# Performance work log

Measured on AMD Instinct MI355X. Metric: run time of the kernel, lower is better.

Reference implementation:

```python
import jax, jax.numpy as jnp
import numpy as np

AT_ID = 5       # tokenizer id of '@'
CITSEG_ID = 7   # tokenizer id of 'CITSEG'


def setup_inputs() -> dict:
    key = jax.random.key(0)
    ks = jax.random.split(key, 12)
    B, S, H = 256, 512, 768
    CIT, D, NC = 750, 1518, 6
    s = lambda n: 1.0 / np.sqrt(n)
    return {
        "tokens": jax.random.randint(ks[0], (B, S), 0, 100),
        "hidden_states": jax.random.normal(ks[1], (B, S, H), jnp.float32),
        "proj_w": jax.random.normal(ks[2], (H, CIT), jnp.float32) * s(H),
        "proj_b": jax.random.normal(ks[3], (CIT,), jnp.float32) * 0.02,
        "enc_w": jax.random.normal(ks[4], (CIT, CIT), jnp.float32) * s(CIT),
        "enc_b": jax.random.normal(ks[5], (CIT,), jnp.float32) * 0.02,
        "w1": jax.random.normal(ks[6], (D, 2 * D), jnp.float32) * s(D),
        "b1": jax.random.normal(ks[7], (2 * D,), jnp.float32) * 0.02,
        "w2": jax.random.normal(ks[8], (2 * D, 2 * D), jnp.float32) * s(2 * D),
        "b2": jax.random.normal(ks[9], (2 * D,), jnp.float32) * 0.02,
        "w3": jax.random.normal(ks[10], (2 * D, NC), jnp.float32) * s(2 * D),
        "b3": jax.random.normal(ks[11], (NC,), jnp.float32) * 0.02,
    }


def _forward(tokens, hidden_states, proj_w, proj_b, enc_w, enc_b,
             w1, b1, w2, b2, w3, b3):
    B, S, H = hidden_states.shape
    idx = jnp.arange(S)[None, :]                       # [1,S]
    BIG = S + 1

    # --- ctx_pooler: masked max over tokens outside the [start,end] '@' span ---
    at_mask = tokens == AT_ID                          # [B,S]
    first = jnp.min(jnp.where(at_mask, idx, BIG), axis=1)            # [B]
    second = jnp.min(jnp.where(at_mask & (idx > first[:, None]), idx, BIG), axis=1)
    ge2 = at_mask.sum(axis=1) >= 2
    start = jnp.where(ge2, first, 0)
    end = jnp.where(ge2, second, S)                    # end=S excludes everything
    keep = (idx < start[:, None]) | (idx > end[:, None])             # [B,S]
    neg = jnp.finfo(hidden_states.dtype).min
    pooled = jnp.max(jnp.where(keep[:, :, None], hidden_states, neg), axis=1)  # [B,H]
    pooled = jnp.where(keep.any(axis=1)[:, None], pooled, 0.0)

    # --- CITSEG token gather + projection (zero row if absent) ---
    c_mask = tokens == CITSEG_ID
    c_first = jnp.min(jnp.where(c_mask, idx, BIG), axis=1)           # [B]
    has_c = c_mask.any(axis=1)
    safe_pos = jnp.minimum(c_first, S - 1)
    cit_h = jnp.take_along_axis(hidden_states, safe_pos[:, None, None], axis=1)[:, 0]  # [B,H]
    cit = (cit_h @ proj_w + proj_b) * has_c[:, None].astype(hidden_states.dtype)       # [B,750]

    # --- citseg_encoder (modeled as Linear 750->750) ---
    cit_enc = cit @ enc_w + enc_b

    # --- MLP head ---
    x = jnp.concatenate([pooled, cit_enc], axis=1)     # [B,1518]
    x = jax.nn.relu(x @ w1 + b1)
    x = jax.nn.relu(x @ w2 + b2)
    return x @ w3 + b3                                 # [B,num_class]


def reference(tokens, hidden_states, proj_w, proj_b, enc_w, enc_b,
              w1, b1, w2, b2, w3, b3):
    return _forward(tokens, hidden_states, proj_w, proj_b, enc_w, enc_b,
                    w1, b1, w2, b2, w3, b3)
```

## Files before the change

kernel.cpp:

```cpp
#include <hip/hip_runtime.h>
#include <hip/hip_bf16.h>

typedef __attribute__((ext_vector_type(8))) short bf16x8;
typedef __attribute__((ext_vector_type(4))) float f32x4;
typedef __attribute__((ext_vector_type(4))) unsigned short u16x4;

#define NEGINF (-3.4028234663852886e38f)

__device__ __forceinline__ unsigned short f2b(float f) {
    union { float f; unsigned u; } x; x.f = f;
    unsigned r = x.u + 0x7FFFu + ((x.u >> 16) & 1u);
    return (unsigned short)(r >> 16);
}
__device__ __forceinline__ float b2f(unsigned short b) {
    union { unsigned u; float f; } x; x.u = ((unsigned)b) << 16;
    return x.f;
}
__device__ __forceinline__ void load_lds16(const void* g, void* l) {
    __builtin_amdgcn_global_load_lds((const __attribute__((address_space(1))) void*)g,
                                     (__attribute__((address_space(3))) void*)l, 16, 0, 0);
}

__global__ __launch_bounds__(192) void scan_cit_k(const int* __restrict__ tokens,
                                                  const float* __restrict__ hs,
                                                  int* __restrict__ meta,
                                                  unsigned short* __restrict__ citA) {
    __shared__ int sm;
    const int S = 512, BIG = 1 << 20;
    int b = blockIdx.x, tid = threadIdx.x;
    if (tid < 64) {
        int l = tid;
        const int* row = tokens + (size_t)b * S;
        int base = l * 8;
        int toks[8];
#pragma unroll
        for (int i = 0; i < 8; ++i) toks[i] = row[base + i];
        int am = 0, cnt = 0, minAt = BIG, minC = BIG;
#pragma unroll
        for (int i = 0; i < 8; ++i) {
            if (toks[i] == 5) { am |= 1 << i; cnt++; if (base + i < minAt) minAt = base + i; }
            if (toks[i] == 7) { if (base + i < minC) minC = base + i; }
        }
        for (int off = 1; off < 64; off <<= 1) {
            minAt = min(minAt, __shfl_xor(minAt, off));
            minC  = min(minC,  __shfl_xor(minC,  off));
            cnt  += __shfl_xor(cnt, off);
        }
        int first = minAt, minAt2 = BIG;
#pragma unroll
        for (int i = 0; i < 8; ++i)
            if ((am >> i) & 1) { int idx = base + i; if (idx > first && idx < minAt2) minAt2 = idx; }
        for (int off = 1; off < 64; off <<= 1) minAt2 = min(minAt2, __shfl_xor(minAt2, off));
        if (l == 0) {
            int ge2 = (cnt >= 2) ? 1 : 0;
            int start = ge2 ? first : 0;
            int end = ge2 ? minAt2 : S;
            int anyKeep = (ge2 && (start > 0 || end < S - 1)) ? 1 : 0;
            int has_c = (minC < S) ? 1 : 0;
            int cpos = min(minC, S - 1);
            int* m = meta + b * 6;
            m[0] = start; m[1] = end; m[2] = cpos; m[3] = has_c; m[4] = anyKeep; m[5] = 0;
            sm = cpos;
        }
    }
    __syncthreads();
    int cpos = sm;
    f32x4 c = *(const f32x4*)(hs + ((size_t)b * 512 + cpos) * 768 + tid * 4);
    u16x4 co;
#pragma unroll
    for (int j = 0; j < 4; ++j) co[j] = f2b(c[j]);
    *(u16x4*)(citA + (size_t)b * 768 + tid * 4) = co;
}

__device__ __forceinline__ void trans32(const float* __restrict__ in, int K, int N,
                                        unsigned short* __restrict__ out, int ldo,
                                        int bx, int by, int tid, float (*tile)[33]) {
    int n0 = bx * 32, k0 = by * 32;
    int tx = tid & 31, ty = tid >> 5;
#pragma unroll
    for (int i = 0; i < 4; ++i) {
        int k = k0 + ty * 4 + i, n = n0 + tx;
        tile[ty * 4 + i][tx] = (k < K && n < N) ? in[(size_t)k * N + n] : 0.f;
    }
    __syncthreads();
    int n = tid >> 3, kc = tid & 7;
    u16x4 o;
#pragma unroll
    for (int q = 0; q < 4; ++q) o[q] = f2b(tile[kc * 4 + q][n]);
    *(u16x4*)(out + (size_t)(n0 + n) * ldo + k0 + kc * 4) = o;
}

__global__ __launch_bounds__(256) void pool_trans_k(
    const float* __restrict__ hs, const int* __restrict__ meta,
    float* __restrict__ part,
    const float* __restrict__ proj_w, const float* __restrict__ enc_w,
    const float* __restrict__ w1, const float* __restrict__ w2,
    unsigned short* __restrict__ projT, unsigned short* __restrict__ encT,
    unsigned short* __restrict__ w1T, unsigned short* __restrict__ w2T) {
    __shared__ float tile[32][33];
    int bid = blockIdx.x, tid = threadIdx.x;
    if (bid < 2048) {
        if (tid >= 192) return;
        int b = bid >> 3, ch = bid & 7;
        int start = meta[b * 6 + 0], end = meta[b * 6 + 1];
        f32x4 m = { NEGINF, NEGINF, NEGINF, NEGINF };
        const float* basep = hs + (size_t)b * 512 * 768 + tid * 4;
        int s0 = ch * 64, hi = s0 + 64;
        int e1 = min(start, hi);
        int s2 = max(end + 1, s0);
#pragma unroll 4
        for (int s = s0; s < e1; ++s) {
            f32x4 v = *(const f32x4*)(basep + (size_t)s * 768);
#pragma unroll
            for (int j = 0; j < 4; ++j) m[j] = fmaxf(m[j], v[j]);
        }
#pragma unroll 4
        for (int s = s2; s < hi; ++s) {
            f32x4 v = *(const f32x4*)(basep + (size_t)s * 768);
#pragma unroll
            for (int j = 0; j < 4; ++j) m[j] = fmaxf(m[j], v[j]);
        }
        *(f32x4*)(part + ((size_t)b * 8 + ch) * 768 + tid * 4) = m;
        return;
    }
    int r = bid - 2048;
    if (r < 576)       { trans32(proj_w, 768, 750, projT, 768, r % 24, r / 24, tid, tile); return; }
    r -= 576;
    if (r < 576)       { trans32(enc_w, 750, 750, encT, 768, r % 24, r / 24, tid, tile); return; }
    r -= 576;
    if (r < 4608)      { trans32(w1, 1518, 3036, w1T, 1536, r % 96, r / 96, tid, tile); return; }
    r -= 4608;
    trans32(w2, 3036, 3036, w2T, 3072, r % 96, r / 96, tid, tile);
}

template<int EPI>
__device__ __forceinline__ void gemm_body(
    const unsigned short* __restrict__ A, int lda,
    const unsigned short* __restrict__ Bt, int ldb,
    const float* __restrict__ bias, const int* __restrict__ meta,
    unsigned short* __restrict__ X, int ldx, int Nreal, int Kp,
    int bx, int by, unsigned short* AsB, unsigned short* BsB) {
    const int tid = threadIdx.x;
    const int wid = tid >> 6, lane = tid & 63;
    const int m0 = by * 64, n0 = bx * 64;
    const int wr = wid >> 1, wc = wid & 1;
    const int c_lin = lane & 15;
    const int rsub = lane >> 4;

    int aoff[4], boff[4], ldst[4];
#pragma unroll
    for (int i = 0; i < 4; ++i) {
        int r = wid * 16 + i * 4 + rsub;
        int csrc = (c_lin ^ (r & 15)) << 3;
        aoff[i] = (m0 + r) * lda + csrc;
        boff[i] = (n0 + r) * ldb + csrc;
        ldst[i] = (wid * 16 + i * 4) * 128;
    }
    int cswz[4];
#pragma unroll
    for (int ks = 0; ks < 4; ++ks) cswz[ks] = ((ks * 4 + (lane >> 4)) ^ c_lin) << 3;
    int arow[2], brow[2];
#pragma unroll
    for (int mi = 0; mi < 2; ++mi) arow[mi] = (wr * 32 + mi * 16 + c_lin) * 128;
#pragma unroll
    for (int nj = 0; nj < 2; ++nj) brow[nj] = (wc * 32 + nj * 16 + c_lin) * 128;

    f32x4 acc[2][2];
    const f32x4 zero = {0.f, 0.f, 0.f, 0.f};
#pragma unroll
    for (int mi = 0; mi < 2; ++mi)
#pragma unroll
        for (int nj = 0; nj < 2; ++nj) acc[mi][nj] = zero;

    auto stage = [&](int nb, int kt) {
#pragma unroll
        for (int i = 0; i < 4; ++i) load_lds16(A + aoff[i] + kt, AsB + nb * 8192 + ldst[i]);
#pragma unroll
        for (int i = 0; i < 4; ++i) load_lds16(Bt + boff[i] + kt, BsB + nb * 8192 + ldst[i]);
    };

    const int nt = Kp >> 7;
    stage(0, 0);
    int cb = 0;
    for (int t = 0; t < nt; ++t) {
        __syncthreads();
        if (t + 1 < nt) stage(cb ^ 1, (t + 1) << 7);
        const unsigned short* as = AsB + cb * 8192;
        const unsigned short* bs = BsB + cb * 8192;
#pragma unroll
        for (int ks = 0; ks < 4; ++ks) {
            bf16x8 af[2], bfr[2];
#pragma unroll
            for (int mi = 0; mi < 2; ++mi) af[mi] = *(const bf16x8*)(as + arow[mi] + cswz[ks]);
#pragma unroll
            for (int nj = 0; nj < 2; ++nj) bfr[nj] = *(const bf16x8*)(bs + brow[nj] + cswz[ks]);
#pragma unroll
            for (int mi = 0; mi < 2; ++mi)
#pragma unroll
                for (int nj = 0; nj < 2; ++nj)
                    acc[mi][nj] = __builtin_amdgcn_mfma_f32_16x16x32_bf16(
                        af[mi], bfr[nj], acc[mi][nj], 0, 0, 0);
        }
        cb ^= 1;
    }
#pragma unroll
    for (int mi = 0; mi < 2; ++mi) {
        int rowb = m0 + wr * 32 + mi * 16 + (lane >> 4) * 4;
#pragma unroll
        for (int nj = 0; nj < 2; ++nj) {
            int col = n0 + wc * 32 + nj * 16 + (lane & 15);
            float bv = (col < Nreal) ? bias[col] : 0.f;
#pragma unroll
            for (int i = 0; i < 4; ++i) {
                int row = rowb + i;
                float v = acc[mi][nj][i] + bv;
                if (EPI == 0) v *= (meta[row * 6 + 3] ? 1.f : 0.f);
                if (EPI == 2) v = fmaxf(v, 0.f);
                if (col >= Nreal) v = 0.f;
                X[(size_t)row * ldx + col] = f2b(v);
            }
        }
    }
}

__global__ __launch_bounds__(256, 2) void pack_g1_k(
    const float* __restrict__ part, const int* __restrict__ meta,
    unsigned short* __restrict__ xA,
    const unsigned short* __restrict__ citA, const unsigned short* __restrict__ projT,
    const float* __restrict__ proj_b, unsigned short* __restrict__ citB) {
    __shared__ __align__(16) unsigned short As[2][64 * 128];
    __shared__ __align__(16) unsigned short Bs[2][64 * 128];
    int bid = blockIdx.x, tid = threadIdx.x;
    if (bid < 256) {
        if (tid >= 192) return;
        int b = bid;
        const float* p = part + (size_t)b * 8 * 768 + tid * 4;
        f32x4 m = *(const f32x4*)p;
#pragma unroll
        for (int ch = 1; ch < 8; ++ch) {
            f32x4 v = *(const f32x4*)(p + (size_t)ch * 768);
#pragma unroll
            for (int j = 0; j < 4; ++j) m[j] = fmaxf(m[j], v[j]);
        }
        if (!meta[b * 6 + 4]) {
            f32x4 z = {0.f, 0.f, 0.f, 0.f};
            m = z;
        }
        u16x4 o;
#pragma unroll
        for (int j = 0; j < 4; ++j) o[j] = f2b(m[j]);
        *(u16x4*)(xA + (size_t)b * 1536 + tid * 4) = o;
        return;
    }
    int r = bid - 256;
    gemm_body<0>(citA, 768, projT, 768, proj_b, meta, citB, 768, 750, 768,
                 r % 12, r / 12, &As[0][0], &Bs[0][0]);
}

template<int EPI>
__global__ __launch_bounds__(256, 2) void gemm_k(
    const unsigned short* __restrict__ A, int lda,
    const unsigned short* __restrict__ Bt, int ldb,
    const float* __restrict__ bias, const int* __restrict__ meta,
    unsigned short* __restrict__ X, int ldx, int Nreal, int Kp) {
    __shared__ __align__(16) unsigned short As[2][64 * 128];
    __shared__ __align__(16) unsigned short Bs[2][64 * 128];
    gemm_body<EPI>(A, lda, Bt, ldb, bias, meta, X, ldx, Nreal, Kp,
                   blockIdx.x, blockIdx.y, &As[0][0], &Bs[0][0]);
}

__global__ __launch_bounds__(256) void out_k(const unsigned short* __restrict__ x2,
                                             const float* __restrict__ w3,
                                             const float* __restrict__ b3,
                                             float* __restrict__ out) {
    int b = blockIdx.x, t = threadIdx.x;
    int wid = t >> 6, lane = t & 63;
    float s[6] = {0.f, 0.f, 0.f, 0.f, 0.f, 0.f};
    const unsigned short* xr = x2 + (size_t)b * 3072;
    for (int k = t; k < 3036; k += 256) {
        float x = b2f(xr[k]);
#pragma unroll
        for (int j = 0; j < 6; ++j) s[j] += x * w3[(size_t)k * 6 + j];
    }
#pragma unroll
    for (int j = 0; j < 6; ++j)
        for (int off = 1; off < 64; off <<= 1) s[j] += __shfl_xor(s[j], off);
    __shared__ float red[4][6];
    if (lane == 0) {
#pragma unroll
        for (int j = 0; j < 6; ++j) red[wid][j] = s[j];
    }
    __syncthreads();
    if (t < 6) out[b * 6 + t] = red[0][t] + red[1][t] + red[2][t] + red[3][t] + b3[t];
}

extern "C" void kernel_launch(void* const* d_in, const int* in_sizes, int n_in,
                              void* d_out, int out_size, void* d_ws, size_t ws_size,
                              hipStream_t stream) {
    const int*   tokens = (const int*)d_in[0];
    const float* hs     = (const float*)d_in[1];
    const float* proj_w = (const float*)d_in[2];
    const float* proj_b = (const float*)d_in[3];
    const float* enc_w  = (const float*)d_in[4];
    const float* enc_b  = (const float*)d_in[5];
    const float* w1 = (const float*)d_in[6];
    const float* b1 = (const float*)d_in[7];
    const float* w2 = (const float*)d_in[8];
    const float* b2 = (const float*)d_in[9];
    const float* w3 = (const float*)d_in[10];
    const float* b3 = (const float*)d_in[11];
    float* out = (float*)d_out;

    char* ws = (char*)d_ws;
    size_t off = 0;
    auto alloc = [&](size_t bytes) {
        void* p = ws + off;
        off = (off + bytes + 255) & ~(size_t)255;
        return p;
    };
    int* meta            = (int*)alloc(256 * 6 * sizeof(int));
    float* part          = (float*)alloc((size_t)256 * 8 * 768 * sizeof(float));
    unsigned short* xA   = (unsigned short*)alloc((size_t)256 * 1536 * 2);
    unsigned short* citA = (unsigned short*)alloc((size_t)256 * 768 * 2);
    unsigned short* citB = (unsigned short*)alloc((size_t)256 * 768 * 2);
    unsigned short* x1   = (unsigned short*)alloc((size_t)256 * 3072 * 2);
    unsigned short* x2   = (unsigned short*)alloc((size_t)256 * 3072 * 2);
    unsigned short* projT= (unsigned short*)alloc((size_t)768 * 768 * 2);
    unsigned short* encT = (unsigned short*)alloc((size_t)768 * 768 * 2);
    unsigned short* w1T  = (unsigned short*)alloc((size_t)3072 * 1536 * 2);
    unsigned short* w2T  = (unsigned short*)alloc((size_t)3072 * 3072 * 2);

    scan_cit_k<<<256, 192, 0, stream>>>(tokens, hs, meta, citA);
    pool_trans_k<<<2048 + 576 + 576 + 4608 + 9216, 256, 0, stream>>>(
        hs, meta, part, proj_w, enc_w, w1, w2, projT, encT, w1T, w2T);
    pack_g1_k<<<304, 256, 0, stream>>>(part, meta, xA, citA, projT, proj_b, citB);
    gemm_k<1><<<dim3(12, 4), 256, 0, stream>>>(citB, 768, encT, 768, enc_b, meta,
                                               xA + 768, 1536, 750, 768);
    gemm_k<2><<<dim3(48, 4), 256, 0, stream>>>(xA, 1536, w1T, 1536, b1, meta,
                                               x1, 3072, 3036, 1536);
    gemm_k<2><<<dim3(48, 4), 256, 0, stream>>>(x1, 3072, w2T, 3072, b2, meta,
                                               x2, 3072, 3036, 3072);
    out_k<<<256, 256, 0, stream>>>(x2, w3, b3, out);
}
```

Before: 153.2 us.

## Fold proj and enc linears into one weight, read fp32 weights directly in GEMMs

Precomputes a combined weight WpeT = proj_w @ enc_w and bias bpe = proj_b @ enc_w + enc_b, so the CITSEG path becomes a single GEMM whose epilogue selects enc_b for rows that have no CITSEG token. The separate transpose-to-bf16 passes over w1 and w2 are removed; the MLP GEMMs now load fp32 weights from global memory, convert them to bf16 in registers and write them swizzled into LDS. Pooling moves to its own kernel. This cuts a large transpose pass and one GEMM launch, at the cost of a weight-product GEMM each call and slower, non-async B-operand staging in the main GEMMs.

```diff
diff --git a/kernel.cpp b/kernel.cpp
--- a/kernel.cpp
+++ b/kernel.cpp
@@ -3,6 +3,7 @@
 
 typedef __attribute__((ext_vector_type(8))) short bf16x8;
 typedef __attribute__((ext_vector_type(4))) float f32x4;
+typedef __attribute__((ext_vector_type(2))) float f32x2;
 typedef __attribute__((ext_vector_type(4))) unsigned short u16x4;
 
 #define NEGINF (-3.4028234663852886e38f)
@@ -20,151 +21,240 @@
     __builtin_amdgcn_global_load_lds((const __attribute__((address_space(1))) void*)g,
                                      (__attribute__((address_space(3))) void*)l, 16, 0, 0);
 }
-
-__global__ __launch_bounds__(192) void scan_cit_k(const int* __restrict__ tokens,
-                                                  const float* __restrict__ hs,
-                                                  int* __restrict__ meta,
-                                                  unsigned short* __restrict__ citA) {
-    __shared__ int sm;
-    const int S = 512, BIG = 1 << 20;
-    int b = blockIdx.x, tid = threadIdx.x;
-    if (tid < 64) {
-        int l = tid;
-        const int* row = tokens + (size_t)b * S;
-        int base = l * 8;
-        int toks[8];
-#pragma unroll
-        for (int i = 0; i < 8; ++i) toks[i] = row[base + i];
-        int am = 0, cnt = 0, minAt = BIG, minC = BIG;
-#pragma unroll
-        for (int i = 0; i < 8; ++i) {
-            if (toks[i] == 5) { am |= 1 << i; cnt++; if (base + i < minAt) minAt = base + i; }
-            if (toks[i] == 7) { if (base + i < minC) minC = base + i; }
-        }
-        for (int off = 1; off < 64; off <<= 1) {
-            minAt = min(minAt, __shfl_xor(minAt, off));
-            minC  = min(minC,  __shfl_xor(minC,  off));
-            cnt  += __shfl_xor(cnt, off);
-        }
-        int first = minAt, minAt2 = BIG;
-#pragma unroll
-        for (int i = 0; i < 8; ++i)
-            if ((am >> i) & 1) { int idx = base + i; if (idx > first && idx < minAt2) minAt2 = idx; }
-        for (int off = 1; off < 64; off <<= 1) minAt2 = min(minAt2, __shfl_xor(minAt2, off));
-        if (l == 0) {
-            int ge2 = (cnt >= 2) ? 1 : 0;
-            int start = ge2 ? first : 0;
-            int end = ge2 ? minAt2 : S;
-            int anyKeep = (ge2 && (start > 0 || end < S - 1)) ? 1 : 0;
-            int has_c = (minC < S) ? 1 : 0;
-            int cpos = min(minC, S - 1);
-            int* m = meta + b * 6;
-            m[0] = start; m[1] = end; m[2] = cpos; m[3] = has_c; m[4] = anyKeep; m[5] = 0;
-            sm = cpos;
-        }
-    }
-    __syncthreads();
-    int cpos = sm;
-    f32x4 c = *(const f32x4*)(hs + ((size_t)b * 512 + cpos) * 768 + tid * 4);
-    u16x4 co;
-#pragma unroll
-    for (int j = 0; j < 4; ++j) co[j] = f2b(c[j]);
-    *(u16x4*)(citA + (size_t)b * 768 + tid * 4) = co;
-}
-
-__device__ __forceinline__ void trans32(const float* __restrict__ in, int K, int N,
-                                        unsigned short* __restrict__ out, int ldo,
-                                        int bx, int by, int tid, float (*tile)[33]) {
-    int n0 = bx * 32, k0 = by * 32;
-    int tx = tid & 31, ty = tid >> 5;
-#pragma unroll
-    for (int i = 0; i < 4; ++i) {
-        int k = k0 + ty * 4 + i, n = n0 + tx;
-        tile[ty * 4 + i][tx] = (k < K && n < N) ? in[(size_t)k * N + n] : 0.f;
-    }
-    __syncthreads();
-    int n = tid >> 3, kc = tid & 7;
-    u16x4 o;
-#pragma unroll
-    for (int q = 0; q < 4; ++q) o[q] = f2b(tile[kc * 4 + q][n]);
-    *(u16x4*)(out + (size_t)(n0 + n) * ldo + k0 + kc * 4) = o;
-}
-
-__global__ __launch_bounds__(256) void pool_trans_k(
-    const float* __restrict__ hs, const int* __restrict__ meta,
-    float* __restrict__ part,
-    const float* __restrict__ proj_w, const float* __restrict__ enc_w,
-    const float* __restrict__ w1, const float* __restrict__ w2,
-    unsigned short* __restrict__ projT, unsigned short* __restrict__ encT,
-    unsigned short* __restrict__ w1T, unsigned short* __restrict__ w2T) {
-    __shared__ float tile[32][33];
-    int bid = blockIdx.x, tid = threadIdx.x;
-    if (bid < 2048) {
-        if (tid >= 192) return;
-        int b = bid >> 3, ch = bid & 7;
-        int start = meta[b * 6 + 0], end = meta[b * 6 + 1];
-        f32x4 m = { NEGINF, NEGINF, NEGINF, NEGINF };
-        const float* basep = hs + (size_t)b * 512 * 768 + tid * 4;
-        int s0 = ch * 64, hi = s0 + 64;
-        int e1 = min(start, hi);
-        int s2 = max(end + 1, s0);
-#pragma unroll 4
-        for (int s = s0; s < e1; ++s) {
-            f32x4 v = *(const f32x4*)(basep + (size_t)s * 768);
-#pragma unroll
-            for (int j = 0; j < 4; ++j) m[j] = fmaxf(m[j], v[j]);
-        }
-#pragma unroll 4
-        for (int s = s2; s < hi; ++s) {
-            f32x4 v = *(const f32x4*)(basep + (size_t)s * 768);
-#pragma unroll
-            for (int j = 0; j < 4; ++j) m[j] = fmaxf(m[j], v[j]);
-        }
-        *(f32x4*)(part + ((size_t)b * 8 + ch) * 768 + tid * 4) = m;
-        return;
-    }
-    int r = bid - 2048;
-    if (r < 576)       { trans32(proj_w, 768, 750, projT, 768, r % 24, r / 24, tid, tile); return; }
-    r -= 576;
-    if (r < 576)       { trans32(enc_w, 750, 750, encT, 768, r % 24, r / 24, tid, tile); return; }
-    r -= 576;
-    if (r < 4608)      { trans32(w1, 1518, 3036, w1T, 1536, r % 96, r / 96, tid, tile); return; }
-    r -= 4608;
-    trans32(w2, 3036, 3036, w2T, 3072, r % 96, r / 96, tid, tile);
-}
-
-template<int EPI>
-__device__ __forceinline__ void gemm_body(
-    const unsigned short* __restrict__ A, int lda,
-    const unsigned short* __restrict__ Bt, int ldb,
-    const float* __restrict__ bias, const int* __restrict__ meta,
-    unsigned short* __restrict__ X, int ldx, int Nreal, int Kp,
-    int bx, int by, unsigned short* AsB, unsigned short* BsB) {
+__device__ __forceinline__ int swzf(int r) { return (r & 15) ^ (r >> 4); }
+
+#define GEMM_COMPUTE(as, bs)                                                        \
+    _Pragma("unroll")                                                               \
+    for (int ks = 0; ks < 4; ++ks) {                                                \
+        int kc = ks * 4 + rsub;                                                     \
+        bf16x8 af[2], bfr[2];                                                       \
+        _Pragma("unroll")                                                           \
+        for (int mi = 0; mi < 2; ++mi) {                                            \
+            int rr = wr * 32 + mi * 16 + c_lin;                                     \
+            af[mi] = *(const bf16x8*)((as) + rr * 128 + ((kc ^ c_lin ^ (wr * 2 + mi)) << 3)); \
+        }                                                                           \
+        _Pragma("unroll")                                                           \
+        for (int nj = 0; nj < 2; ++nj) {                                            \
+            int rr = wc * 32 + nj * 16 + c_lin;                                     \
+            bfr[nj] = *(const bf16x8*)((bs) + rr * 128 + ((kc ^ c_lin ^ (wc * 2 + nj)) << 3)); \
+        }                                                                           \
+        _Pragma("unroll")                                                           \
+        for (int mi = 0; mi < 2; ++mi)                                              \
+            _Pragma("unroll")                                                       \
+            for (int nj = 0; nj < 2; ++nj)                                          \
+                acc[mi][nj] = __builtin_amdgcn_mfma_f32_16x16x32_bf16(              \
+                    af[mi], bfr[nj], acc[mi][nj], 0, 0, 0);                         \
+    }
+
+__device__ __forceinline__ void wpe_body(const float* __restrict__ proj,
+                                         const float* __restrict__ enc,
+                                         unsigned short* __restrict__ WpeT,
+                                         int bx, int by,
+                                         unsigned short* AsB, unsigned short* BsB) {
+    const int KR = 750;
     const int tid = threadIdx.x;
     const int wid = tid >> 6, lane = tid & 63;
     const int m0 = by * 64, n0 = bx * 64;
     const int wr = wid >> 1, wc = wid & 1;
-    const int c_lin = lane & 15;
-    const int rsub = lane >> 4;
+    const int c_lin = lane & 15, rsub = lane >> 4;
+    const int tn = (tid & 15) * 4, tc = tid >> 4;
+
+    f32x4 acc[2][2];
+    const f32x4 zero = {0.f, 0.f, 0.f, 0.f};
+#pragma unroll
+    for (int mi = 0; mi < 2; ++mi)
+#pragma unroll
+        for (int nj = 0; nj < 2; ++nj) acc[mi][nj] = zero;
+
+    f32x4 vb[8];
+    auto stageA = [&](int nb, int kt) {
+#pragma unroll
+        for (int p = 0; p < 4; ++p) {
+            int r = p * 16 + tc;
+            float v[8];
+#pragma unroll
+            for (int e = 0; e < 4; ++e) {
+                int d = kt + (tid & 15) * 8 + e * 2;
+                int dcl = min(d, KR - 2);
+                f32x2 t2 = *(const f32x2*)(proj + (size_t)(m0 + r) * KR + dcl);
+                v[e * 2]     = (d < KR) ? t2[0] : 0.f;
+                v[e * 2 + 1] = (d + 1 < KR) ? t2[1] : 0.f;
+            }
+            bf16x8 w;
+#pragma unroll
+            for (int e = 0; e < 8; ++e) w[e] = (short)f2b(v[e]);
+            int c = tid & 15;
+            *(bf16x8*)(AsB + nb * 8192 + r * 128 + ((c ^ swzf(r)) << 3)) = w;
+        }
+    };
+    auto loadB = [&](int kt) {
+        int nbl = n0 + tn;
+        int n1 = min(nbl, 748), n2 = min(nbl + 2, 748);
+#pragma unroll
+        for (int p = 0; p < 8; ++p) {
+            int kg = min(kt + tc * 8 + p, KR - 1);
+            const float* rowp = enc + (size_t)kg * KR;
+            f32x2 a = *(const f32x2*)(rowp + n1);
+            f32x2 b = *(const f32x2*)(rowp + n2);
+            f32x4 t; t[0] = a[0]; t[1] = a[1]; t[2] = b[0]; t[3] = b[1];
+            vb[p] = t;
+        }
+    };
+    auto writeB = [&](int nb) {
+#pragma unroll
+        for (int q = 0; q < 4; ++q) {
+            int row = tn + q;
+            bf16x8 w;
+#pragma unroll
+            for (int p = 0; p < 8; ++p) w[p] = (short)f2b(vb[p][q]);
+            *(bf16x8*)(BsB + nb * 8192 + row * 128 + ((tc ^ swzf(row)) << 3)) = w;
+        }
+    };
+
+    const int nt = 6;
+    stageA(0, 0); loadB(0); writeB(0);
+    int cb = 0;
+    for (int t = 0; t < nt; ++t) {
+        __syncthreads();
+        if (t + 1 < nt) { stageA(cb ^ 1, (t + 1) << 7); loadB((t + 1) << 7); }
+        const unsigned short* as = AsB + cb * 8192;
+        const unsigned short* bs = BsB + cb * 8192;
+        GEMM_COMPUTE(as, bs)
+        if (t + 1 < nt) writeB(cb ^ 1);
+        cb ^= 1;
+    }
+#pragma unroll
+    for (int mi = 0; mi < 2; ++mi) {
+        int hb = m0 + wr * 32 + mi * 16 + rsub * 4;
+#pragma unroll
+        for (int nj = 0; nj < 2; ++nj) {
+            int j = n0 + wc * 32 + nj * 16 + c_lin;
+#pragma unroll
+            for (int i = 0; i < 4; ++i)
+                WpeT[(size_t)j * 768 + hb + i] = f2b(acc[mi][nj][i]);
+        }
+    }
+}
+
+__global__ __launch_bounds__(256, 2) void k1_prep_k(
+    const int* __restrict__ tokens, const float* __restrict__ hs,
+    int* __restrict__ meta, unsigned short* __restrict__ citA,
+    const float* __restrict__ proj_w, const float* __restrict__ enc_w,
+    const float* __restrict__ proj_b, const float* __restrict__ enc_b,
+    unsigned short* __restrict__ WpeT, float* __restrict__ bpe) {
+    __shared__ __align__(16) unsigned short As[2][8192];
+    __shared__ __align__(16) unsigned short Bs[2][8192];
+    int bid = blockIdx.x, tid = threadIdx.x;
+    if (bid < 256) {
+        __shared__ int sm;
+        const int S = 512, BIG = 1 << 20;
+        int b = bid;
+        if (tid < 64) {
+            int l = tid;
+            const int* row = tokens + (size_t)b * S;
+            int base = l * 8;
+            int toks[8];
+#pragma unroll
+            for (int i = 0; i < 8; ++i) toks[i] = row[base + i];
+            int am = 0, cnt = 0, minAt = BIG, minC = BIG;
+#pragma unroll
+            for (int i = 0; i < 8; ++i) {
+                if (toks[i] == 5) { am |= 1 << i; cnt++; if (base + i < minAt) minAt = base + i; }
+                if (toks[i] == 7) { if (base + i < minC) minC = base + i; }
+            }
+            for (int off = 1; off < 64; off <<= 1) {
+                minAt = min(minAt, __shfl_xor(minAt, off));
+                minC  = min(minC,  __shfl_xor(minC,  off));
+                cnt  += __shfl_xor(cnt, off);
+            }
+            int first = minAt, minAt2 = BIG;
+#pragma unroll
+            for (int i = 0; i < 8; ++i)
+                if ((am >> i) & 1) { int idx = base + i; if (idx > first && idx < minAt2) minAt2 = idx; }
+            for (int off = 1; off < 64; off <<= 1) minAt2 = min(minAt2, __shfl_xor(minAt2, off));
+            if (l == 0) {
+                int ge2 = (cnt >= 2) ? 1 : 0;
+                int start = ge2 ? first : 0;
+                int end = ge2 ? minAt2 : S;
+                int anyKeep = (ge2 && (start > 0 || end < S - 1)) ? 1 : 0;
+                int has_c = (minC < S) ? 1 : 0;
+                int cpos = min(minC, S - 1);
+                int* m = meta + b * 6;
+                m[0] = start; m[1] = end; m[2] = cpos; m[3] = has_c; m[4] = anyKeep; m[5] = 0;
+                sm = cpos;
+            }
+        }
+        __syncthreads();
+        if (tid < 192) {
+            int cpos = sm;
+            f32x4 c = *(const f32x4*)(hs + ((size_t)b * 512 + cpos) * 768 + tid * 4);
+            u16x4 co;
+#pragma unroll
+            for (int j = 0; j < 4; ++j) co[j] = f2b(c[j]);
+            *(u16x4*)(citA + (size_t)b * 768 + tid * 4) = co;
+        }
+        return;
+    }
+    if (bid < 400) {
+        int r = bid - 256;
+        wpe_body(proj_w, enc_w, WpeT, r % 12, r / 12, &As[0][0], &Bs[0][0]);
+        return;
+    }
+    int j = (bid - 400) * 256 + tid;
+    if (j < 750) {
+        float a = enc_b[j];
+        for (int d = 0; d < 750; ++d) a += proj_b[d] * enc_w[(size_t)d * 750 + j];
+        bpe[j] = a;
+    }
+}
+
+__global__ __launch_bounds__(192) void pool_k(const float* __restrict__ hs,
+                                              const int* __restrict__ meta,
+                                              float* __restrict__ part) {
+    int b = blockIdx.x >> 3, ch = blockIdx.x & 7;
+    int start = meta[b * 6 + 0], end = meta[b * 6 + 1];
+    int t = threadIdx.x;
+    f32x4 m = { NEGINF, NEGINF, NEGINF, NEGINF };
+    const float* basep = hs + (size_t)b * 512 * 768 + t * 4;
+    int s0 = ch * 64, hi = s0 + 64;
+    int e1 = min(start, hi);
+    int s2 = max(end + 1, s0);
+#pragma unroll 4
+    for (int s = s0; s < e1; ++s) {
+        f32x4 v = *(const f32x4*)(basep + (size_t)s * 768);
+#pragma unroll
+        for (int j = 0; j < 4; ++j) m[j] = fmaxf(m[j], v[j]);
+    }
+#pragma unroll 4
+    for (int s = s2; s < hi; ++s) {
+        f32x4 v = *(const f32x4*)(basep + (size_t)s * 768);
+#pragma unroll
+        for (int j = 0; j < 4; ++j) m[j] = fmaxf(m[j], v[j]);
+    }
+    *(f32x4*)(part + ((size_t)b * 8 + ch) * 768 + t * 4) = m;
+}
+
+__device__ __forceinline__ void g12_body(
+    const unsigned short* __restrict__ A, const unsigned short* __restrict__ Bt,
+    const float* __restrict__ bpe, const float* __restrict__ encb,
+    const int* __restrict__ meta, unsigned short* __restrict__ X,
+    int bx, int by, unsigned short* AsB, unsigned short* BsB) {
+    const int lda = 768, ldb = 768, ldx = 1536, Nreal = 750;
+    const int tid = threadIdx.x;
+    const int wid = tid >> 6, lane = tid & 63;
+    const int m0 = by * 64, n0 = bx * 64;
+    const int wr = wid >> 1, wc = wid & 1;
+    const int c_lin = lane & 15, rsub = lane >> 4;
 
     int aoff[4], boff[4], ldst[4];
 #pragma unroll
     for (int i = 0; i < 4; ++i) {
         int r = wid * 16 + i * 4 + rsub;
-        int csrc = (c_lin ^ (r & 15)) << 3;
+        int csrc = (c_lin ^ swzf(r)) << 3;
         aoff[i] = (m0 + r) * lda + csrc;
         boff[i] = (n0 + r) * ldb + csrc;
         ldst[i] = (wid * 16 + i * 4) * 128;
     }
-    int cswz[4];
-#pragma unroll
-    for (int ks = 0; ks < 4; ++ks) cswz[ks] = ((ks * 4 + (lane >> 4)) ^ c_lin) << 3;
-    int arow[2], brow[2];
-#pragma unroll
-    for (int mi = 0; mi < 2; ++mi) arow[mi] = (wr * 32 + mi * 16 + c_lin) * 128;
-#pragma unroll
-    for (int nj = 0; nj < 2; ++nj) brow[nj] = (wc * 32 + nj * 16 + c_lin) * 128;
-
     f32x4 acc[2][2];
     const f32x4 zero = {0.f, 0.f, 0.f, 0.f};
 #pragma unroll
@@ -178,8 +268,7 @@
 #pragma unroll
         for (int i = 0; i < 4; ++i) load_lds16(Bt + boff[i] + kt, BsB + nb * 8192 + ldst[i]);
     };
-
-    const int nt = Kp >> 7;
+    const int nt = 6;
     stage(0, 0);
     int cb = 0;
     for (int t = 0; t < nt; ++t) {
@@ -187,35 +276,22 @@
         if (t + 1 < nt) stage(cb ^ 1, (t + 1) << 7);
         const unsigned short* as = AsB + cb * 8192;
         const unsigned short* bs = BsB + cb * 8192;
-#pragma unroll
-        for (int ks = 0; ks < 4; ++ks) {
-            bf16x8 af[2], bfr[2];
-#pragma unroll
-            for (int mi = 0; mi < 2; ++mi) af[mi] = *(const bf16x8*)(as + arow[mi] + cswz[ks]);
-#pragma unroll
-            for (int nj = 0; nj < 2; ++nj) bfr[nj] = *(const bf16x8*)(bs + brow[nj] + cswz[ks]);
-#pragma unroll
-            for (int mi = 0; mi < 2; ++mi)
-#pragma unroll
-                for (int nj = 0; nj < 2; ++nj)
-                    acc[mi][nj] = __builtin_amdgcn_mfma_f32_16x16x32_bf16(
-                        af[mi], bfr[nj], acc[mi][nj], 0, 0, 0);
-        }
+        GEMM_COMPUTE(as, bs)
         cb ^= 1;
     }
 #pragma unroll
     for (int mi = 0; mi < 2; ++mi) {
-        int rowb = m0 + wr * 32 + mi * 16 + (lane >> 4) * 4;
+        int rowb = m0 + wr * 32 + mi * 16 + rsub * 4;
 #pragma unroll
         for (int nj = 0; nj < 2; ++nj) {
-            int col = n0 + wc * 32 + nj * 16 + (lane & 15);
-            float bv = (col < Nreal) ? bias[col] : 0.f;
+            int col = n0 + wc * 32 + nj * 16 + c_lin;
+            float bv = (col < Nreal) ? bpe[col] : 0.f;
+            float ev = (col < Nreal) ? encb[col] : 0.f;
 #pragma unroll
             for (int i = 0; i < 4; ++i) {
                 int row = rowb + i;
                 float v = acc[mi][nj][i] + bv;
-                if (EPI == 0) v *= (meta[row * 6 + 3] ? 1.f : 0.f);
-                if (EPI == 2) v = fmaxf(v, 0.f);
+                v = meta[row * 6 + 3] ? v : ev;
                 if (col >= Nreal) v = 0.f;
                 X[(size_t)row * ldx + col] = f2b(v);
             }
@@ -223,13 +299,13 @@
     }
 }
 
-__global__ __launch_bounds__(256, 2) void pack_g1_k(
+__global__ __launch_bounds__(256, 2) void pack_g12_k(
     const float* __restrict__ part, const int* __restrict__ meta,
     unsigned short* __restrict__ xA,
-    const unsigned short* __restrict__ citA, const unsigned short* __restrict__ projT,
-    const float* __restrict__ proj_b, unsigned short* __restrict__ citB) {
-    __shared__ __align__(16) unsigned short As[2][64 * 128];
-    __shared__ __align__(16) unsigned short Bs[2][64 * 128];
+    const unsigned short* __restrict__ citA, const unsigned short* __restrict__ WpeT,
+    const float* __restrict__ bpe, const float* __restrict__ encb) {
+    __shared__ __align__(16) unsigned short As[2][8192];
+    __shared__ __align__(16) unsigned short Bs[2][8192];
     int bid = blockIdx.x, tid = threadIdx.x;
     if (bid < 256) {
         if (tid >= 192) return;
@@ -253,20 +329,90 @@
         return;
     }
     int r = bid - 256;
-    gemm_body<0>(citA, 768, projT, 768, proj_b, meta, citB, 768, 750, 768,
-                 r % 12, r / 12, &As[0][0], &Bs[0][0]);
-}
-
-template<int EPI>
-__global__ __launch_bounds__(256, 2) void gemm_k(
-    const unsigned short* __restrict__ A, int lda,
-    const unsigned short* __restrict__ Bt, int ldb,
-    const float* __restrict__ bias, const int* __restrict__ meta,
-    unsigned short* __restrict__ X, int ldx, int Nreal, int Kp) {
-    __shared__ __align__(16) unsigned short As[2][64 * 128];
-    __shared__ __align__(16) unsigned short Bs[2][64 * 128];
-    gemm_body<EPI>(A, lda, Bt, ldb, bias, meta, X, ldx, Nreal, Kp,
-                   blockIdx.x, blockIdx.y, &As[0][0], &Bs[0][0]);
+    g12_body(citA, WpeT, bpe, encb, meta, xA + 768, r % 12, r / 12, &As[0][0], &Bs[0][0]);
+}
+
+__global__ __launch_bounds__(256, 2) void gemm_relu_k(
+    const unsigned short* __restrict__ A, int lda, int Kp,
+    const float* __restrict__ B, int ldn, int Kreal,
+    const float* __restrict__ bias,
+    unsigned short* __restrict__ X, int ldx, int Nreal) {
+    __shared__ __align__(16) unsigned short As[2][8192];
+    __shared__ __align__(16) unsigned short Bs[2][8192];
+    unsigned short* AsB = &As[0][0];
+    unsigned short* BsB = &Bs[0][0];
+    const int tid = threadIdx.x;
+    const int wid = tid >> 6, lane = tid & 63;
+    const int m0 = blockIdx.y * 64, n0 = blockIdx.x * 64;
+    const int wr = wid >> 1, wc = wid & 1;
+    const int c_lin = lane & 15, rsub = lane >> 4;
+    const int tn = (tid & 15) * 4, tc = tid >> 4;
+    const int nbase = min(n0 + tn, ldn - 4);
+
+    int aoff[4], ldstA[4];
+#pragma unroll
+    for (int i = 0; i < 4; ++i) {
+        int r = wid * 16 + i * 4 + rsub;
+        aoff[i] = (m0 + r) * lda + ((c_lin ^ swzf(r)) << 3);
+        ldstA[i] = (wid * 16 + i * 4) * 128;
+    }
+    f32x4 acc[2][2];
+    const f32x4 zero = {0.f, 0.f, 0.f, 0.f};
+#pragma unroll
+    for (int mi = 0; mi < 2; ++mi)
+#pragma unroll
+        for (int nj = 0; nj < 2; ++nj) acc[mi][nj] = zero;
+
+    f32x4 vb[8];
+    auto stageA = [&](int nb, int kt) {
+#pragma unroll
+        for (int i = 0; i < 4; ++i) load_lds16(A + aoff[i] + kt, AsB + nb * 8192 + ldstA[i]);
+    };
+    auto loadB = [&](int kt) {
+#pragma unroll
+        for (int p = 0; p < 8; ++p) {
+            int kg = min(kt + tc * 8 + p, Kreal - 1);
+            vb[p] = *(const f32x4*)(B + (size_t)kg * ldn + nbase);
+        }
+    };
+    auto writeB = [&](int nb) {
+#pragma unroll
+        for (int q = 0; q < 4; ++q) {
+            int row = tn + q;
+            bf16x8 w;
+#pragma unroll
+            for (int p = 0; p < 8; ++p) w[p] = (short)f2b(vb[p][q]);
+            *(bf16x8*)(BsB + nb * 8192 + row * 128 + ((tc ^ swzf(row)) << 3)) = w;
+        }
+    };
+
+    const int nt = Kp >> 7;
+    stageA(0, 0); loadB(0); writeB(0);
+    int cb = 0;
+    for (int t = 0; t < nt; ++t) {
+        __syncthreads();
+        if (t + 1 < nt) { stageA(cb ^ 1, (t + 1) << 7); loadB((t + 1) << 7); }
+        const unsigned short* as = AsB + cb * 8192;
+        const unsigned short* bs = BsB + cb * 8192;
+        GEMM_COMPUTE(as, bs)
+        if (t + 1 < nt) writeB(cb ^ 1);
+        cb ^= 1;
+    }
+#pragma unroll
+    for (int mi = 0; mi < 2; ++mi) {
+        int rowb = m0 + wr * 32 + mi * 16 + rsub * 4;
+#pragma unroll
+        for (int nj = 0; nj < 2; ++nj) {
+            int col = n0 + wc * 32 + nj * 16 + c_lin;
+            float bv = (col < Nreal) ? bias[col] : 0.f;
+#pragma unroll
+            for (int i = 0; i < 4; ++i) {
+                float v = fmaxf(acc[mi][nj][i] + bv, 0.f);
+                if (col >= Nreal) v = 0.f;
+                X[(size_t)(rowb + i) * ldx + col] = f2b(v);
+            }
+        }
+    }
 }
 
 __global__ __launch_bounds__(256) void out_k(const unsigned short* __restrict__ x2,
@@ -322,23 +468,18 @@
     float* part          = (float*)alloc((size_t)256 * 8 * 768 * sizeof(float));
     unsigned short* xA   = (unsigned short*)alloc((size_t)256 * 1536 * 2);
     unsigned short* citA = (unsigned short*)alloc((size_t)256 * 768 * 2);
-    unsigned short* citB = (unsigned short*)alloc((size_t)256 * 768 * 2);
     unsigned short* x1   = (unsigned short*)alloc((size_t)256 * 3072 * 2);
     unsigned short* x2   = (unsigned short*)alloc((size_t)256 * 3072 * 2);
-    unsigned short* projT= (unsigned short*)alloc((size_t)768 * 768 * 2);
-    unsigned short* encT = (unsigned short*)alloc((size_t)768 * 768 * 2);
-    unsigned short* w1T  = (unsigned short*)alloc((size_t)3072 * 1536 * 2);
-    unsigned short* w2T  = (unsigned short*)alloc((size_t)3072 * 3072 * 2);
-
-    scan_cit_k<<<256, 192, 0, stream>>>(tokens, hs, meta, citA);
-    pool_trans_k<<<2048 + 576 + 576 + 4608 + 9216, 256, 0, stream>>>(
-        hs, meta, part, proj_w, enc_w, w1, w2, projT, encT, w1T, w2T);
-    pack_g1_k<<<304, 256, 0, stream>>>(part, meta, xA, citA, projT, proj_b, citB);
-    gemm_k<1><<<dim3(12, 4), 256, 0, stream>>>(citB, 768, encT, 768, enc_b, meta,
-                                               xA + 768, 1536, 750, 768);
-    gemm_k<2><<<dim3(48, 4), 256, 0, stream>>>(xA, 1536, w1T, 1536, b1, meta,
-                                               x1, 3072, 3036, 1536);
-    gemm_k<2><<<dim3(48, 4), 256, 0, stream>>>(x1, 3072, w2T, 3072, b2, meta,
-                                               x2, 3072, 3036, 3072);
+    unsigned short* WpeT = (unsigned short*)alloc((size_t)768 * 768 * 2);
+    float* bpe           = (float*)alloc(768 * sizeof(float));
+
+    k1_prep_k<<<403, 256, 0, stream>>>(tokens, hs, meta, citA, proj_w, enc_w,
+                                       proj_b, enc_b, WpeT, bpe);
+    pool_k<<<2048, 192, 0, stream>>>(hs, meta, part);
+    pack_g12_k<<<304, 256, 0, stream>>>(part, meta, xA, citA, WpeT, bpe, enc_b);
+    gemm_relu_k<<<dim3(48, 4), 256, 0, stream>>>(xA, 1536, 1536, w1, 3036, 1518,
+                                                 b1, x1, 3072, 3036);
+    gemm_relu_k<<<dim3(48, 4), 256, 0, stream>>>(x1, 3072, 3072, w2, 3036, 3036,
+                                                 b2, x2, 3072, 3036);
     out_k<<<256, 256, 0, stream>>>(x2, w3, b3, out);
 }
```

New measurement: 198.1 us. 1.29x slower.

## Fuse scan into pooling kernel and merge tail GEMMs into persistent grid-barrier kernel

Applied to the files above, without the earlier changes.

Removes the separate token-scan kernel. Each pooling block now recomputes the '@' span with wave ballots, and dedicated blocks in the same launch write the meta array and gather the CITSEG row. The projection, encoder, two MLP GEMMs and the output layer are merged into one 304-block kernel separated by software grid barriers. This cuts seven launches to two plus a memset and removes inter-kernel gaps. It adds a spin-wait barrier that needs all 304 blocks resident at once, and redundant token scanning in every pooling block.

```diff
diff --git a/kernel.cpp b/kernel.cpp
--- a/kernel.cpp
+++ b/kernel.cpp
@@ -6,6 +6,7 @@
 typedef __attribute__((ext_vector_type(4))) unsigned short u16x4;
 
 #define NEGINF (-3.4028234663852886e38f)
+#define BIGP (1 << 20)
 
 __device__ __forceinline__ unsigned short f2b(float f) {
     union { float f; unsigned u; } x; x.f = f;
@@ -21,21 +22,87 @@
                                      (__attribute__((address_space(3))) void*)l, 16, 0, 0);
 }
 
-__global__ __launch_bounds__(192) void scan_cit_k(const int* __restrict__ tokens,
-                                                  const float* __restrict__ hs,
-                                                  int* __restrict__ meta,
-                                                  unsigned short* __restrict__ citA) {
-    __shared__ int sm;
-    const int S = 512, BIG = 1 << 20;
-    int b = blockIdx.x, tid = threadIdx.x;
-    if (tid < 64) {
-        int l = tid;
+__device__ __forceinline__ void trans32(const float* __restrict__ in, int K, int N,
+                                        unsigned short* __restrict__ out, int ldo,
+                                        int bx, int by, int tid, float (*tile)[33]) {
+    int n0 = bx * 32, k0 = by * 32;
+    int tx = tid & 31, ty = tid >> 5;
+#pragma unroll
+    for (int i = 0; i < 4; ++i) {
+        int k = k0 + ty * 4 + i, n = n0 + tx;
+        tile[ty * 4 + i][tx] = (k < K && n < N) ? in[(size_t)k * N + n] : 0.f;
+    }
+    __syncthreads();
+    int n = tid >> 3, kc = tid & 7;
+    u16x4 o;
+#pragma unroll
+    for (int q = 0; q < 4; ++q) o[q] = f2b(tile[kc * 4 + q][n]);
+    *(u16x4*)(out + (size_t)(n0 + n) * ldo + k0 + kc * 4) = o;
+}
+
+__global__ __launch_bounds__(256) void pool_mega_k(
+    const int* __restrict__ tokens, const float* __restrict__ hs,
+    int* __restrict__ meta, unsigned short* __restrict__ citA,
+    float* __restrict__ part,
+    const float* __restrict__ proj_w, const float* __restrict__ enc_w,
+    const float* __restrict__ w1, const float* __restrict__ w2,
+    unsigned short* __restrict__ projT, unsigned short* __restrict__ encT,
+    unsigned short* __restrict__ w1T, unsigned short* __restrict__ w2T) {
+    __shared__ float tile[32][33];
+    int bid = blockIdx.x, tid = threadIdx.x;
+    if (bid < 2048) {
+        if (tid >= 192) return;
+        int b = bid >> 3, ch = bid & 7;
+        int lane = tid & 63;
+        const int* row = tokens + (size_t)b * 512;
+        int first = BIGP, second = BIGP;
+#pragma unroll
+        for (int c = 0; c < 8; ++c) {
+            int tok = row[c * 64 + lane];
+            unsigned long long m = __ballot(tok == 5);
+            if (m) {
+                int base = c * 64;
+                if (first == BIGP) {
+                    first = base + (int)__ffsll(m) - 1;
+                    unsigned long long m2 = m & (m - 1);
+                    if (m2) second = base + (int)__ffsll(m2) - 1;
+                } else if (second == BIGP) {
+                    second = base + (int)__ffsll(m) - 1;
+                }
+            }
+        }
+        int start, end;
+        if (second < BIGP) { start = first; end = second; }
+        else               { start = 0;     end = 512;    }
+        f32x4 m = { NEGINF, NEGINF, NEGINF, NEGINF };
+        const float* basep = hs + (size_t)b * 512 * 768 + tid * 4;
+        int s0 = ch * 64, hi = s0 + 64;
+        int e1 = min(start, hi);
+        int s2 = max(end + 1, s0);
+#pragma unroll 4
+        for (int s = s0; s < e1; ++s) {
+            f32x4 v = *(const f32x4*)(basep + (size_t)s * 768);
+#pragma unroll
+            for (int j = 0; j < 4; ++j) m[j] = fmaxf(m[j], v[j]);
+        }
+#pragma unroll 4
+        for (int s = s2; s < hi; ++s) {
+            f32x4 v = *(const f32x4*)(basep + (size_t)s * 768);
+#pragma unroll
+            for (int j = 0; j < 4; ++j) m[j] = fmaxf(m[j], v[j]);
+        }
+        *(f32x4*)(part + ((size_t)b * 8 + ch) * 768 + tid * 4) = m;
+        return;
+    }
+    if (bid < 2112) {
+        const int S = 512;
+        int b = (bid - 2048) * 4 + (tid >> 6), l = tid & 63;
         const int* row = tokens + (size_t)b * S;
         int base = l * 8;
         int toks[8];
 #pragma unroll
         for (int i = 0; i < 8; ++i) toks[i] = row[base + i];
-        int am = 0, cnt = 0, minAt = BIG, minC = BIG;
+        int am = 0, cnt = 0, minAt = BIGP, minC = BIGP;
 #pragma unroll
         for (int i = 0; i < 8; ++i) {
             if (toks[i] == 5) { am |= 1 << i; cnt++; if (base + i < minAt) minAt = base + i; }
@@ -46,7 +113,7 @@
             minC  = min(minC,  __shfl_xor(minC,  off));
             cnt  += __shfl_xor(cnt, off);
         }
-        int first = minAt, minAt2 = BIG;
+        int first = minAt, minAt2 = BIGP;
 #pragma unroll
         for (int i = 0; i < 8; ++i)
             if ((am >> i) & 1) { int idx = base + i; if (idx > first && idx < minAt2) minAt2 = idx; }
@@ -60,75 +127,34 @@
             int cpos = min(minC, S - 1);
             int* m = meta + b * 6;
             m[0] = start; m[1] = end; m[2] = cpos; m[3] = has_c; m[4] = anyKeep; m[5] = 0;
-            sm = cpos;
-        }
-    }
-    __syncthreads();
-    int cpos = sm;
-    f32x4 c = *(const f32x4*)(hs + ((size_t)b * 512 + cpos) * 768 + tid * 4);
-    u16x4 co;
-#pragma unroll
-    for (int j = 0; j < 4; ++j) co[j] = f2b(c[j]);
-    *(u16x4*)(citA + (size_t)b * 768 + tid * 4) = co;
-}
-
-__device__ __forceinline__ void trans32(const float* __restrict__ in, int K, int N,
-                                        unsigned short* __restrict__ out, int ldo,
-                                        int bx, int by, int tid, float (*tile)[33]) {
-    int n0 = bx * 32, k0 = by * 32;
-    int tx = tid & 31, ty = tid >> 5;
-#pragma unroll
-    for (int i = 0; i < 4; ++i) {
-        int k = k0 + ty * 4 + i, n = n0 + tx;
-        tile[ty * 4 + i][tx] = (k < K && n < N) ? in[(size_t)k * N + n] : 0.f;
-    }
-    __syncthreads();
-    int n = tid >> 3, kc = tid & 7;
-    u16x4 o;
-#pragma unroll
-    for (int q = 0; q < 4; ++q) o[q] = f2b(tile[kc * 4 + q][n]);
-    *(u16x4*)(out + (size_t)(n0 + n) * ldo + k0 + kc * 4) = o;
-}
-
-__global__ __launch_bounds__(256) void pool_trans_k(
-    const float* __restrict__ hs, const int* __restrict__ meta,
-    float* __restrict__ part,
-    const float* __restrict__ proj_w, const float* __restrict__ enc_w,
-    const float* __restrict__ w1, const float* __restrict__ w2,
-    unsigned short* __restrict__ projT, unsigned short* __restrict__ encT,
-    unsigned short* __restrict__ w1T, unsigned short* __restrict__ w2T) {
-    __shared__ float tile[32][33];
-    int bid = blockIdx.x, tid = threadIdx.x;
-    if (bid < 2048) {
+        }
+        return;
+    }
+    if (bid < 2368) {
         if (tid >= 192) return;
-        int b = bid >> 3, ch = bid & 7;
-        int start = meta[b * 6 + 0], end = meta[b * 6 + 1];
-        f32x4 m = { NEGINF, NEGINF, NEGINF, NEGINF };
-        const float* basep = hs + (size_t)b * 512 * 768 + tid * 4;
-        int s0 = ch * 64, hi = s0 + 64;
-        int e1 = min(start, hi);
-        int s2 = max(end + 1, s0);
-#pragma unroll 4
-        for (int s = s0; s < e1; ++s) {
-            f32x4 v = *(const f32x4*)(basep + (size_t)s * 768);
-#pragma unroll
-            for (int j = 0; j < 4; ++j) m[j] = fmaxf(m[j], v[j]);
-        }
-#pragma unroll 4
-        for (int s = s2; s < hi; ++s) {
-            f32x4 v = *(const f32x4*)(basep + (size_t)s * 768);
-#pragma unroll
-            for (int j = 0; j < 4; ++j) m[j] = fmaxf(m[j], v[j]);
-        }
-        *(f32x4*)(part + ((size_t)b * 8 + ch) * 768 + tid * 4) = m;
+        int b = bid - 2112, lane = tid & 63;
+        const int* row = tokens + (size_t)b * 512;
+        int minC = BIGP;
+#pragma unroll
+        for (int c = 0; c < 8; ++c) {
+            int tok = row[c * 64 + lane];
+            unsigned long long m = __ballot(tok == 7);
+            if (minC == BIGP && m) minC = c * 64 + (int)__ffsll(m) - 1;
+        }
+        int cpos = min(minC, 511);
+        f32x4 cv = *(const f32x4*)(hs + ((size_t)b * 512 + cpos) * 768 + tid * 4);
+        u16x4 co;
+#pragma unroll
+        for (int j = 0; j < 4; ++j) co[j] = f2b(cv[j]);
+        *(u16x4*)(citA + (size_t)b * 768 + tid * 4) = co;
         return;
     }
-    int r = bid - 2048;
-    if (r < 576)       { trans32(proj_w, 768, 750, projT, 768, r % 24, r / 24, tid, tile); return; }
+    int r = bid - 2368;
+    if (r < 576)  { trans32(proj_w, 768, 750, projT, 768, r % 24, r / 24, tid, tile); return; }
     r -= 576;
-    if (r < 576)       { trans32(enc_w, 750, 750, encT, 768, r % 24, r / 24, tid, tile); return; }
+    if (r < 576)  { trans32(enc_w, 750, 750, encT, 768, r % 24, r / 24, tid, tile); return; }
     r -= 576;
-    if (r < 4608)      { trans32(w1, 1518, 3036, w1T, 1536, r % 96, r / 96, tid, tile); return; }
+    if (r < 4608) { trans32(w1, 1518, 3036, w1T, 1536, r % 96, r / 96, tid, tile); return; }
     r -= 4608;
     trans32(w2, 3036, 3036, w2T, 3072, r % 96, r / 96, tid, tile);
 }
@@ -158,7 +184,7 @@
     }
     int cswz[4];
 #pragma unroll
-    for (int ks = 0; ks < 4; ++ks) cswz[ks] = ((ks * 4 + (lane >> 4)) ^ c_lin) << 3;
+    for (int ks = 0; ks < 4; ++ks) cswz[ks] = ((ks * 4 + rsub) ^ c_lin) << 3;
     int arow[2], brow[2];
 #pragma unroll
     for (int mi = 0; mi < 2; ++mi) arow[mi] = (wr * 32 + mi * 16 + c_lin) * 128;
@@ -203,12 +229,13 @@
         }
         cb ^= 1;
     }
+    __syncthreads();
 #pragma unroll
     for (int mi = 0; mi < 2; ++mi) {
-        int rowb = m0 + wr * 32 + mi * 16 + (lane >> 4) * 4;
+        int rowb = m0 + wr * 32 + mi * 16 + rsub * 4;
 #pragma unroll
         for (int nj = 0; nj < 2; ++nj) {
-            int col = n0 + wc * 32 + nj * 16 + (lane & 15);
+            int col = n0 + wc * 32 + nj * 16 + c_lin;
             float bv = (col < Nreal) ? bias[col] : 0.f;
 #pragma unroll
             for (int i = 0; i < 4; ++i) {
@@ -223,75 +250,94 @@
     }
 }
 
-__global__ __launch_bounds__(256, 2) void pack_g1_k(
+__device__ __forceinline__ void gbar(int* cnt, int nblk) {
+    __syncthreads();
+    if (threadIdx.x == 0) {
+        __threadfence();
+        atomicAdd(cnt, 1);
+        while (__hip_atomic_load(cnt, __ATOMIC_ACQUIRE, __HIP_MEMORY_SCOPE_AGENT) < nblk)
+            __builtin_amdgcn_s_sleep(8);
+    }
+    __syncthreads();
+}
+
+__global__ __launch_bounds__(256, 2) void tail_k(
     const float* __restrict__ part, const int* __restrict__ meta,
     unsigned short* __restrict__ xA,
-    const unsigned short* __restrict__ citA, const unsigned short* __restrict__ projT,
-    const float* __restrict__ proj_b, unsigned short* __restrict__ citB) {
-    __shared__ __align__(16) unsigned short As[2][64 * 128];
-    __shared__ __align__(16) unsigned short Bs[2][64 * 128];
+    const unsigned short* __restrict__ citA,
+    const unsigned short* __restrict__ projT, const float* __restrict__ proj_b,
+    unsigned short* __restrict__ citB,
+    const unsigned short* __restrict__ encT, const float* __restrict__ enc_b,
+    const unsigned short* __restrict__ w1T, const float* __restrict__ b1,
+    unsigned short* __restrict__ x1,
+    const unsigned short* __restrict__ w2T, const float* __restrict__ b2,
+    unsigned short* __restrict__ x2,
+    const float* __restrict__ w3, const float* __restrict__ b3,
+    float* __restrict__ out, int* __restrict__ bar) {
+    __shared__ __align__(16) unsigned short As[2][8192];
+    __shared__ __align__(16) unsigned short Bs[2][8192];
+    __shared__ float red[4][6];
+    const int NB = 304;
     int bid = blockIdx.x, tid = threadIdx.x;
+
     if (bid < 256) {
-        if (tid >= 192) return;
+        if (tid < 192) {
+            int b = bid;
+            const float* p = part + (size_t)b * 8 * 768 + tid * 4;
+            f32x4 m = *(const f32x4*)p;
+#pragma unroll
+            for (int ch = 1; ch < 8; ++ch) {
+                f32x4 v = *(const f32x4*)(p + (size_t)ch * 768);
+#pragma unroll
+                for (int j = 0; j < 4; ++j) m[j] = fmaxf(m[j], v[j]);
+            }
+            if (!meta[b * 6 + 4]) {
+                f32x4 z = {0.f, 0.f, 0.f, 0.f};
+                m = z;
+            }
+            u16x4 o;
+#pragma unroll
+            for (int j = 0; j < 4; ++j) o[j] = f2b(m[j]);
+            *(u16x4*)(xA + (size_t)b * 1536 + tid * 4) = o;
+        }
+    } else {
+        int r = bid - 256;
+        gemm_body<0>(citA, 768, projT, 768, proj_b, meta, citB, 768, 750, 768,
+                     r % 12, r / 12, &As[0][0], &Bs[0][0]);
+    }
+    gbar(bar + 0 * 16, NB);
+    if (bid < 48)
+        gemm_body<1>(citB, 768, encT, 768, enc_b, meta, xA + 768, 1536, 750, 768,
+                     bid % 12, bid / 12, &As[0][0], &Bs[0][0]);
+    gbar(bar + 1 * 16, NB);
+    if (bid < 192)
+        gemm_body<2>(xA, 1536, w1T, 1536, b1, meta, x1, 3072, 3036, 1536,
+                     bid % 48, bid / 48, &As[0][0], &Bs[0][0]);
+    gbar(bar + 2 * 16, NB);
+    if (bid < 192)
+        gemm_body<2>(x1, 3072, w2T, 3072, b2, meta, x2, 3072, 3036, 3072,
+                     bid % 48, bid / 48, &As[0][0], &Bs[0][0]);
+    gbar(bar + 3 * 16, NB);
+    if (bid < 256) {
         int b = bid;
-        const float* p = part + (size_t)b * 8 * 768 + tid * 4;
-        f32x4 m = *(const f32x4*)p;
-#pragma unroll
-        for (int ch = 1; ch < 8; ++ch) {
-            f32x4 v = *(const f32x4*)(p + (size_t)ch * 768);
-#pragma unroll
-            for (int j = 0; j < 4; ++j) m[j] = fmaxf(m[j], v[j]);
-        }
-        if (!meta[b * 6 + 4]) {
-            f32x4 z = {0.f, 0.f, 0.f, 0.f};
-            m = z;
-        }
-        u16x4 o;
-#pragma unroll
-        for (int j = 0; j < 4; ++j) o[j] = f2b(m[j]);
-        *(u16x4*)(xA + (size_t)b * 1536 + tid * 4) = o;
-        return;
-    }
-    int r = bid - 256;
-    gemm_body<0>(citA, 768, projT, 768, proj_b, meta, citB, 768, 750, 768,
-                 r % 12, r / 12, &As[0][0], &Bs[0][0]);
-}
-
-template<int EPI>
-__global__ __launch_bounds__(256, 2) void gemm_k(
-    const unsigned short* __restrict__ A, int lda,
-    const unsigned short* __restrict__ Bt, int ldb,
-    const float* __restrict__ bias, const int* __restrict__ meta,
-    unsigned short* __restrict__ X, int ldx, int Nreal, int Kp) {
-    __shared__ __align__(16) unsigned short As[2][64 * 128];
-    __shared__ __align__(16) unsigned short Bs[2][64 * 128];
-    gemm_body<EPI>(A, lda, Bt, ldb, bias, meta, X, ldx, Nreal, Kp,
-                   blockIdx.x, blockIdx.y, &As[0][0], &Bs[0][0]);
-}
-
-__global__ __launch_bounds__(256) void out_k(const unsigned short* __restrict__ x2,
-                                             const float* __restrict__ w3,
-                                             const float* __restrict__ b3,
-                                             float* __restrict__ out) {
-    int b = blockIdx.x, t = threadIdx.x;
-    int wid = t >> 6, lane = t & 63;
-    float s[6] = {0.f, 0.f, 0.f, 0.f, 0.f, 0.f};
-    const unsigned short* xr = x2 + (size_t)b * 3072;
-    for (int k = t; k < 3036; k += 256) {
-        float x = b2f(xr[k]);
-#pragma unroll
-        for (int j = 0; j < 6; ++j) s[j] += x * w3[(size_t)k * 6 + j];
-    }
-#pragma unroll
-    for (int j = 0; j < 6; ++j)
-        for (int off = 1; off < 64; off <<= 1) s[j] += __shfl_xor(s[j], off);
-    __shared__ float red[4][6];
-    if (lane == 0) {
-#pragma unroll
-        for (int j = 0; j < 6; ++j) red[wid][j] = s[j];
-    }
-    __syncthreads();
-    if (t < 6) out[b * 6 + t] = red[0][t] + red[1][t] + red[2][t] + red[3][t] + b3[t];
+        int wid = tid >> 6, lane = tid & 63;
+        float s[6] = {0.f, 0.f, 0.f, 0.f, 0.f, 0.f};
+        const unsigned short* xr = x2 + (size_t)b * 3072;
+        for (int k = tid; k < 3036; k += 256) {
+            float x = b2f(xr[k]);
+#pragma unroll
+            for (int j = 0; j < 6; ++j) s[j] += x * w3[(size_t)k * 6 + j];
+        }
+#pragma unroll
+        for (int j = 0; j < 6; ++j)
+            for (int off = 1; off < 64; off <<= 1) s[j] += __shfl_xor(s[j], off);
+        if (lane == 0) {
+#pragma unroll
+            for (int j = 0; j < 6; ++j) red[wid][j] = s[j];
+        }
+        __syncthreads();
+        if (tid < 6) out[b * 6 + tid] = red[0][tid] + red[1][tid] + red[2][tid] + red[3][tid] + b3[tid];
+    }
 }
 
 extern "C" void kernel_launch(void* const* d_in, const int* in_sizes, int n_in,
@@ -329,16 +375,14 @@
     unsigned short* encT = (unsigned short*)alloc((size_t)768 * 768 * 2);
     unsigned short* w1T  = (unsigned short*)alloc((size_t)3072 * 1536 * 2);
     unsigned short* w2T  = (unsigned short*)alloc((size_t)3072 * 3072 * 2);
-
-    scan_cit_k<<<256, 192, 0, stream>>>(tokens, hs, meta, citA);
-    pool_trans_k<<<2048 + 576 + 576 + 4608 + 9216, 256, 0, stream>>>(
-        hs, meta, part, proj_w, enc_w, w1, w2, projT, encT, w1T, w2T);
-    pack_g1_k<<<304, 256, 0, stream>>>(part, meta, xA, citA, projT, proj_b, citB);
-    gemm_k<1><<<dim3(12, 4), 256, 0, stream>>>(citB, 768, encT, 768, enc_b, meta,
-                                               xA + 768, 1536, 750, 768);
-    gemm_k<2><<<dim3(48, 4), 256, 0, stream>>>(xA, 1536, w1T, 1536, b1, meta,
-                                               x1, 3072, 3036, 1536);
-    gemm_k<2><<<dim3(48, 4), 256, 0, stream>>>(x1, 3072, w2T, 3072, b2, meta,
-                                               x2, 3072, 3036, 3072);
-    out_k<<<256, 256, 0, stream>>>(x2, w3, b3, out);
-}
+    int* bar             = (int*)alloc(4 * 16 * sizeof(int));
+
+    hipMemsetAsync(bar, 0, 4 * 16 * sizeof(int), stream);
+
+    pool_mega_k<<<17344, 256, 0, stream>>>(tokens, hs, meta, citA, part,
+                                           proj_w, enc_w, w1, w2,
+                                           projT, encT, w1T, w2T);
+    tail_k<<<304, 256, 0, stream>>>(part, meta, xA, citA, projT, proj_b, citB,
+                                    encT, enc_b, w1T, b1, x1, w2T, b2, x2,
+                                    w3, b3, out, bar);
+}
```

After: 365.4 us. +138.5%, slower.
